# Optimization experiments

Hardware: AMD Instinct MI355X
Metric: run time of the kernel (lower is better)

The kernel has to match this reference:

```python
import jax, jax.numpy as jnp
import numpy as np

NUM_CLASSES = 9
B, H, W = 8, 768, 768


def setup_inputs() -> dict:
    key = jax.random.key(0)
    k1, k2 = jax.random.split(key)
    masks = jax.random.randint(k1, (B, H, W), 0, NUM_CLASSES, dtype=jnp.int32)
    outputs = jax.random.normal(k2, (B, NUM_CLASSES, H, W), dtype=jnp.float32)
    return {"masks": masks, "outputs": outputs}


def reference(masks, outputs):
    b, c, h, w = outputs.shape
    k = NUM_CLASSES
    eye = jnp.eye(k, dtype=outputs.dtype)
    smooth = eye * 0.9 + (1.0 - eye) * (0.1 / 8.0)  # [K, K] smoothed targets

    # Fused segment-mean over all pixels: segment id = batch*K + class label.
    feats = jnp.transpose(outputs, (0, 2, 3, 1)).reshape(b * h * w, c)  # [BHW, C]
    ids = (jnp.arange(b, dtype=jnp.int32)[:, None, None] * k + masks).reshape(-1)
    sums = jax.ops.segment_sum(feats, ids, num_segments=b * k).reshape(b, k, c)
    counts = jax.ops.segment_sum(
        jnp.ones((b * h * w,), outputs.dtype), ids, num_segments=b * k
    ).reshape(b, k)

    # torch.unique(mask)[1:] drops label 0 (background); mask absent classes.
    protos = sums[:, 1:, :] / jnp.maximum(counts[:, 1:, None], 1.0)  # [B, K-1, C]
    present = counts[:, 1:] > 0  # [B, K-1]

    logp = jax.nn.log_softmax(protos, axis=-1)  # [B, K-1, C]
    tgt = smooth[1:]  # [K-1, C] soft targets for classes 1..K-1
    per_proto = -jnp.sum(tgt[None, :, :] * logp, axis=-1)  # [B, K-1]

    n_present = jnp.maximum(jnp.sum(present).astype(outputs.dtype), 1.0)
    loss = jnp.sum(jnp.where(present, per_proto, 0.0)) / n_present
    return loss
```

## Files before the change

### kernel.cpp

```cpp
#include <hip/hip_runtime.h>
#include <hip/hip_bf16.h>
#include <math.h>

#define NB 8
#define NC 9
#define PIXELS (768*768)
#define BLOCK 256
#define PPT 12
#define CHUNK_PX (BLOCK * PPT)
#define NCHUNK (PIXELS / CHUNK_PX)
#define NITER (PPT / 4)
#define NWAVE (BLOCK / 64)
#define GRID (NB * NCHUNK)
#define SLOT 80

__global__ __launch_bounds__(BLOCK)
void accum_kernel(const int* __restrict__ masks,
                  const float* __restrict__ outputs,
                  float* __restrict__ partial)
{
    int blk = blockIdx.x;
    int chunk = blk % NCHUNK;
    int b = blk / NCHUNK;
    int t = threadIdx.x;
    int wave = t >> 6;
    int lane = t & 63;

    const int4* __restrict__ m4 =
        (const int4*)(masks + (size_t)b * PIXELS + (size_t)chunk * CHUNK_PX);
    int4 m[NITER];
    #pragma unroll
    for (int i = 0; i < NITER; ++i) m[i] = m4[t + i * BLOCK];

    __shared__ float red[NC][NWAVE][8];
    __shared__ float red_c[NWAVE][8];

    {
        int cnt[8];
        #pragma unroll
        for (int k = 0; k < 8; ++k) cnt[k] = 0;
        #pragma unroll
        for (int i = 0; i < NITER; ++i) {
            #pragma unroll
            for (int k = 1; k <= 8; ++k) {
                cnt[k - 1] += __popcll(__ballot(m[i].x == k));
                cnt[k - 1] += __popcll(__ballot(m[i].y == k));
                cnt[k - 1] += __popcll(__ballot(m[i].z == k));
                cnt[k - 1] += __popcll(__ballot(m[i].w == k));
            }
        }
        if (lane == 0) {
            #pragma unroll
            for (int k = 0; k < 8; ++k) red_c[wave][k] = (float)cnt[k];
        }
    }

    const float* outbase = outputs + (size_t)b * NC * PIXELS + (size_t)chunk * CHUNK_PX;

    const int p = lane & 1;
    const int q = (lane >> 1) & 1;
    const int r = (lane >> 2) & 1;

    #pragma unroll
    for (int c = 0; c < NC; ++c) {
        const float4* o4 = (const float4*)(outbase + (size_t)c * PIXELS);
        float4 buf[NITER];
        #pragma unroll
        for (int i = 0; i < NITER; ++i) buf[i] = o4[t + i * BLOCK];

        float s[8];
        #pragma unroll
        for (int k = 0; k < 8; ++k) s[k] = 0.f;

        #pragma unroll
        for (int i = 0; i < NITER; ++i) {
            float4 v = buf[i];
            #pragma unroll
            for (int k = 1; k <= 8; ++k) {
                float a = s[k - 1];
                a += (m[i].x == k) ? v.x : 0.f;
                a += (m[i].y == k) ? v.y : 0.f;
                a += (m[i].z == k) ? v.z : 0.f;
                a += (m[i].w == k) ? v.w : 0.f;
                s[k - 1] = a;
            }
        }

        float u[4];
        #pragma unroll
        for (int j = 0; j < 4; ++j) {
            float x = p ? s[j] : s[j + 4];
            float y = __shfl_xor(x, 1, 64);
            u[j] = (p ? s[j + 4] : s[j]) + y;
        }
        float v2[2];
        #pragma unroll
        for (int j = 0; j < 2; ++j) {
            float x = q ? u[j] : u[j + 2];
            float y = __shfl_xor(x, 2, 64);
            v2[j] = (q ? u[j + 2] : u[j]) + y;
        }
        float w;
        {
            float x = r ? v2[0] : v2[1];
            float y = __shfl_xor(x, 4, 64);
            w = (r ? v2[1] : v2[0]) + y;
        }
        w += __shfl_xor(w, 8, 64);
        w += __shfl_xor(w, 16, 64);
        w += __shfl_xor(w, 32, 64);

        if (lane < 8) {
            int cls = (p << 2) | (q << 1) | r;
            red[c][wave][cls] = w;
        }
    }

    __syncthreads();

    if (t < NC * 8) {
        int c = t >> 3;
        int k = t & 7;
        float tot = 0.f;
        #pragma unroll
        for (int w = 0; w < NWAVE; ++w) tot += red[c][w][k];
        partial[(size_t)blk * SLOT + c * 8 + k] = tot;
    } else if (t < NC * 8 + 8) {
        int k = t - NC * 8;
        float tot = 0.f;
        #pragma unroll
        for (int w = 0; w < NWAVE; ++w) tot += red_c[w][k];
        partial[(size_t)blk * SLOT + 72 + k] = tot;
    }
}

__global__ __launch_bounds__(1024)
void finalize_kernel(const float* __restrict__ partial,
                     float* __restrict__ out)
{
    __shared__ float tot[NB][SLOT];
    int t = threadIdx.x;

    if (t < NB * SLOT) {
        int b = t / SLOT;
        int col = t % SLOT;
        const float* p = partial + (size_t)b * NCHUNK * SLOT + col;
        float s = 0.f;
        #pragma unroll 8
        for (int blk = 0; blk < NCHUNK; ++blk) s += p[(size_t)blk * SLOT];
        tot[b][col] = s;
    }
    __syncthreads();

    if (t < 64) {
        int b = t >> 3;
        int cls = t & 7;

        float cntv = tot[b][72 + cls];
        float denom = fmaxf(cntv, 1.0f);

        float pr[NC];
        float mx = -INFINITY;
        #pragma unroll
        for (int c = 0; c < NC; ++c) {
            pr[c] = tot[b][c * 8 + cls] / denom;
            mx = fmaxf(mx, pr[c]);
        }
        float se = 0.f;
        #pragma unroll
        for (int c = 0; c < NC; ++c) se += expf(pr[c] - mx);
        float lse = logf(se);

        float per = 0.f;
        #pragma unroll
        for (int c = 0; c < NC; ++c) {
            float tgt = (c == cls + 1) ? 0.9f : 0.0125f;
            per -= tgt * (pr[c] - mx - lse);
        }

        bool present = cntv > 0.f;
        float val = present ? per : 0.f;
        float np  = present ? 1.f : 0.f;
        #pragma unroll
        for (int off = 32; off > 0; off >>= 1) {
            val += __shfl_down(val, off, 64);
            np  += __shfl_down(np,  off, 64);
        }
        if (t == 0) out[0] = val / fmaxf(np, 1.f);
    }
}

extern "C" void kernel_launch(void* const* d_in, const int* in_sizes, int n_in,
                              void* d_out, int out_size, void* d_ws, size_t ws_size,
                              hipStream_t stream) {
    const int*   masks   = (const int*)d_in[0];
    const float* outputs = (const float*)d_in[1];
    float* partial = (float*)d_ws;

    accum_kernel<<<GRID, BLOCK, 0, stream>>>(masks, outputs, partial);
    finalize_kernel<<<1, 1024, 0, stream>>>(partial, (float*)d_out);
}
```

Measured before the change: 258.1 us.

## Shrink per-thread pixel chunk, disable channel unroll, raise occupancy hint

Each thread now covers 8 pixels instead of 12, which gives more blocks. The channel loop is no longer unrolled, and launch bounds ask for 8 blocks per CU to cut register pressure and raise occupancy. With the channel loop rolled, the loads for all 9 channels can no longer be issued ahead of the math, so the kernel leans on more resident waves to hide memory latency. The finalize kernel reads more partial slots, since the grid grows from 1536 to 2304 blocks.

Result: slower. 265.7 us (+2.9%).

```diff
diff --git a/kernel.cpp b/kernel.cpp
--- a/kernel.cpp
+++ b/kernel.cpp
@@ -1,20 +1,46 @@
 #include <hip/hip_runtime.h>
-#include <hip/hip_bf16.h>
 #include <math.h>
 
 #define NB 8
 #define NC 9
 #define PIXELS (768*768)
 #define BLOCK 256
-#define PPT 12
+#define PPT 8
 #define CHUNK_PX (BLOCK * PPT)
 #define NCHUNK (PIXELS / CHUNK_PX)
-#define NITER (PPT / 4)
 #define NWAVE (BLOCK / 64)
 #define GRID (NB * NCHUNK)
 #define SLOT 80
 
-__global__ __launch_bounds__(BLOCK)
+__device__ __forceinline__ float butterfly8(const float s[8], int p, int q, int r)
+{
+    float u[4];
+    #pragma unroll
+    for (int j = 0; j < 4; ++j) {
+        float x = p ? s[j] : s[j + 4];
+        float y = __shfl_xor(x, 1, 64);
+        u[j] = (p ? s[j + 4] : s[j]) + y;
+    }
+    float v2[2];
+    #pragma unroll
+    for (int j = 0; j < 2; ++j) {
+        float x = q ? u[j] : u[j + 2];
+        float y = __shfl_xor(x, 2, 64);
+        v2[j] = (q ? u[j + 2] : u[j]) + y;
+    }
+    float w;
+    {
+        float x = r ? v2[0] : v2[1];
+        float y = __shfl_xor(x, 4, 64);
+        w = (r ? v2[1] : v2[0]) + y;
+    }
+    w += __shfl_xor(w, 8, 64);
+    w += __shfl_xor(w, 16, 64);
+    w += __shfl_xor(w, 32, 64);
+    return w;
+}
+
+__global__ __launch_bounds__(BLOCK, 8)
 void accum_kernel(const int* __restrict__ masks,
                   const float* __restrict__ outputs,
                   float* __restrict__ partial)
@@ -28,26 +54,30 @@
 
     const int4* __restrict__ m4 =
         (const int4*)(masks + (size_t)b * PIXELS + (size_t)chunk * CHUNK_PX);
-    int4 m[NITER];
-    #pragma unroll
-    for (int i = 0; i < NITER; ++i) m[i] = m4[t + i * BLOCK];
+    int4 m0 = m4[t];
+    int4 m1 = m4[t + BLOCK];
 
     __shared__ float red[NC][NWAVE][8];
     __shared__ float red_c[NWAVE][8];
 
+    const int p = lane & 1;
+    const int q = (lane >> 1) & 1;
+    const int r = (lane >> 2) & 1;
+
     {
         int cnt[8];
         #pragma unroll
         for (int k = 0; k < 8; ++k) cnt[k] = 0;
         #pragma unroll
-        for (int i = 0; i < NITER; ++i) {
-            #pragma unroll
-            for (int k = 1; k <= 8; ++k) {
-                cnt[k - 1] += __popcll(__ballot(m[i].x == k));
-                cnt[k - 1] += __popcll(__ballot(m[i].y == k));
-                cnt[k - 1] += __popcll(__ballot(m[i].z == k));
-                cnt[k - 1] += __popcll(__ballot(m[i].w == k));
-            }
+        for (int k = 1; k <= 8; ++k) {
+            cnt[k - 1] += __popcll(__ballot(m0.x == k));
+            cnt[k - 1] += __popcll(__ballot(m0.y == k));
+            cnt[k - 1] += __popcll(__ballot(m0.z == k));
+            cnt[k - 1] += __popcll(__ballot(m0.w == k));
+            cnt[k - 1] += __popcll(__ballot(m1.x == k));
+            cnt[k - 1] += __popcll(__ballot(m1.y == k));
+            cnt[k - 1] += __popcll(__ballot(m1.z == k));
+            cnt[k - 1] += __popcll(__ballot(m1.w == k));
         }
         if (lane == 0) {
             #pragma unroll
@@ -57,63 +87,32 @@
 
     const float* outbase = outputs + (size_t)b * NC * PIXELS + (size_t)chunk * CHUNK_PX;
 
-    const int p = lane & 1;
-    const int q = (lane >> 1) & 1;
-    const int r = (lane >> 2) & 1;
-
-    #pragma unroll
+    #pragma unroll 1
     for (int c = 0; c < NC; ++c) {
         const float4* o4 = (const float4*)(outbase + (size_t)c * PIXELS);
-        float4 buf[NITER];
-        #pragma unroll
-        for (int i = 0; i < NITER; ++i) buf[i] = o4[t + i * BLOCK];
+        float4 v0 = o4[t];
+        float4 v1 = o4[t + BLOCK];
 
         float s[8];
         #pragma unroll
         for (int k = 0; k < 8; ++k) s[k] = 0.f;
 
         #pragma unroll
-        for (int i = 0; i < NITER; ++i) {
-            float4 v = buf[i];
-            #pragma unroll
-            for (int k = 1; k <= 8; ++k) {
-                float a = s[k - 1];
-                a += (m[i].x == k) ? v.x : 0.f;
-                a += (m[i].y == k) ? v.y : 0.f;
-                a += (m[i].z == k) ? v.z : 0.f;
-                a += (m[i].w == k) ? v.w : 0.f;
-                s[k - 1] = a;
-            }
-        }
-
-        float u[4];
-        #pragma unroll
-        for (int j = 0; j < 4; ++j) {
-            float x = p ? s[j] : s[j + 4];
-            float y = __shfl_xor(x, 1, 64);
-            u[j] = (p ? s[j + 4] : s[j]) + y;
-        }
-        float v2[2];
-        #pragma unroll
-        for (int j = 0; j < 2; ++j) {
-            float x = q ? u[j] : u[j + 2];
-            float y = __shfl_xor(x, 2, 64);
-            v2[j] = (q ? u[j + 2] : u[j]) + y;
-        }
-        float w;
-        {
-            float x = r ? v2[0] : v2[1];
-            float y = __shfl_xor(x, 4, 64);
-            w = (r ? v2[1] : v2[0]) + y;
-        }
-        w += __shfl_xor(w, 8, 64);
-        w += __shfl_xor(w, 16, 64);
-        w += __shfl_xor(w, 32, 64);
-
-        if (lane < 8) {
-            int cls = (p << 2) | (q << 1) | r;
-            red[c][wave][cls] = w;
-        }
+        for (int k = 1; k <= 8; ++k) {
+            float a = s[k - 1];
+            a += (m0.x == k) ? v0.x : 0.f;
+            a += (m0.y == k) ? v0.y : 0.f;
+            a += (m0.z == k) ? v0.z : 0.f;
+            a += (m0.w == k) ? v0.w : 0.f;
+            a += (m1.x == k) ? v1.x : 0.f;
+            a += (m1.y == k) ? v1.y : 0.f;
+            a += (m1.z == k) ? v1.z : 0.f;
+            a += (m1.w == k) ? v1.w : 0.f;
+            s[k - 1] = a;
+        }
+
+        float w = butterfly8(s, p, q, r);
+        if (lane < 8) red[c][wave][(p << 2) | (q << 1) | r] = w;
     }
 
     __syncthreads();
```
